# Performance work log

Hardware: AMD Instinct MI355X
Metric: run time of the kernel (lower is better)

The kernel has to match this reference:

```python
import math
import jax, jax.numpy as jnp
import numpy as np

N = 20000      # nodes
E = 320000     # edges
D_IN = 256
D_OUT = 256
H = 8
DK = D_OUT // H  # 32


def setup_inputs() -> dict:
    key = jax.random.key(0)
    ks = jax.random.split(key, 16)
    h = jax.random.normal(ks[0], (N, D_IN), dtype=jnp.float32)
    src = jax.random.randint(ks[1], (E,), 0, N, dtype=jnp.int32)
    dst = jax.random.randint(ks[2], (E,), 0, N, dtype=jnp.int32)
    s = 1.0 / math.sqrt(D_IN)
    Wk = jax.random.uniform(ks[3], (D_OUT, D_IN), jnp.float32, -s, s)
    bk = jnp.zeros((D_OUT,), jnp.float32)
    Wq = jax.random.uniform(ks[4], (D_OUT, D_IN), jnp.float32, -s, s)
    bq = jnp.zeros((D_OUT,), jnp.float32)
    Wv = jax.random.uniform(ks[5], (D_OUT, D_IN), jnp.float32, -s, s)
    bv = jnp.zeros((D_OUT,), jnp.float32)
    so = 1.0 / math.sqrt(D_OUT)
    Wa = jax.random.uniform(ks[6], (D_OUT, D_OUT), jnp.float32, -so, so)
    ba = jnp.zeros((D_OUT,), jnp.float32)
    # xavier_uniform over [n_rel=1, H, DK, DK]; fan_in = fan_out = DK
    bound = math.sqrt(6.0 / (DK + DK))
    rel_att = jax.random.uniform(ks[7], (H, DK, DK), jnp.float32, -bound, bound)
    rel_msg = jax.random.uniform(ks[8], (H, DK, DK), jnp.float32, -bound, bound)
    rel_pri = jnp.ones((H,), jnp.float32)
    skip = jnp.ones((), jnp.float32)
    return {"h": h, "src": src, "dst": dst, "Wk": Wk, "bk": bk, "Wq": Wq,
            "bq": bq, "Wv": Wv, "bv": bv, "Wa": Wa, "ba": ba,
            "rel_att": rel_att, "rel_msg": rel_msg, "rel_pri": rel_pri,
            "skip": skip}


def reference(h, src, dst, Wk, bk, Wq, bq, Wv, bv, Wa, ba, rel_att, rel_msg, rel_pri, skip):
    n = h.shape[0]
    sqrt_dk = math.sqrt(DK)
    # per-node projections, [N, H, DK]
    k = (h @ Wk.T + bk).reshape(n, H, DK)
    q = (h @ Wq.T + bq).reshape(n, H, DK)
    v = (h @ Wv.T + bv).reshape(n, H, DK)
    # relation-specific transforms (single relation, index 0)
    k = jnp.einsum('nhd,hde->nhe', k, rel_att)
    v = jnp.einsum('nhd,hde->nhe', v, rel_msg)
    # edge-wise dot-product score: v_dot_u(q_dst, k_src) -> [E, H]
    score = jnp.einsum('ehd,ehd->eh', q[dst], k[src]) * rel_pri / sqrt_dk
    # edge softmax normalized by dst
    m = jax.ops.segment_max(score, dst, num_segments=n)          # [N, H]
    ex = jnp.exp(score - m[dst])
    z = jax.ops.segment_sum(ex, dst, num_segments=n)             # [N, H]
    attn = ex / z[dst]                                           # [E, H]
    # weighted message aggregation: sum_e attn * v_src -> [N, H, DK]
    agg = jax.ops.segment_sum(v[src] * attn[:, :, None], dst, num_segments=n)
    t = agg.reshape(n, D_OUT)
    trans = t @ Wa.T + ba                                        # dropout = eval identity
    alpha = jax.nn.sigmoid(skip)
    return trans * alpha + h * (1.0 - alpha)
```

## Files before the change

kernel.cpp:

```cpp
#include <hip/hip_runtime.h>
#include <hip/hip_bf16.h>
#include <math.h>


#define NN   20000
#define NE   320000
#define MPAD 20096
#define DSTRIDE 96

typedef unsigned short u16;
typedef unsigned char  u8;
typedef __bf16 bf16x8 __attribute__((ext_vector_type(8)));
typedef u16    u16x8  __attribute__((ext_vector_type(8)));
typedef float  f32x4  __attribute__((ext_vector_type(4)));

__device__ __forceinline__ float bf2f(u16 x) {
    union { float f; unsigned u; } c; c.u = ((unsigned)x) << 16; return c.f;
}
__device__ __forceinline__ u16 f2bf(float f) {
    union { float f; unsigned u; } c; c.f = f;
    unsigned r = c.u + 0x7fffu + ((c.u >> 16) & 1u);
    return (u16)(r >> 16);
}

#if __has_builtin(__builtin_amdgcn_cvt_pk_fp8_f32) && __has_builtin(__builtin_amdgcn_cvt_pk_f32_fp8)
#define HWFP8 1
#else
#define HWFP8 0
#endif

__device__ __forceinline__ u8 f2fp8(float x) {
#if HWFP8
    return (u8)(__builtin_amdgcn_cvt_pk_fp8_f32(x, x, 0, false) & 0xff);
#else
    if (x != x) return 0x7f;
    unsigned sg = (x < 0.f) ? 0x80u : 0u;
    float a = fabsf(x); if (a > 448.f) a = 448.f;
    if (a < 0.015625f) {
        int m = (int)rintf(a * 512.f);
        if (m > 7) return (u8)(sg | 0x08);
        return (u8)(sg | m);
    }
    int e; (void)frexpf(a, &e);
    int p = e - 1;
    float mant = a * exp2f((float)(-p));
    int m = (int)rintf((mant - 1.f) * 8.f);
    int ef = p + 7;
    if (m == 8) { m = 0; ef++; }
    if (ef > 15) { ef = 15; m = 6; }
    return (u8)(sg | (ef << 3) | m);
#endif
}

__device__ __forceinline__ void fp8x4_dec(unsigned w, float* o) {
#if HWFP8
    auto lo = __builtin_amdgcn_cvt_pk_f32_fp8(w, false);
    auto hi = __builtin_amdgcn_cvt_pk_f32_fp8(w, true);
    o[0] = lo[0]; o[1] = lo[1]; o[2] = hi[0]; o[3] = hi[1];
#else
    #pragma unroll
    for (int j = 0; j < 4; ++j) {
        u8 b = (w >> (8 * j)) & 0xff;
        unsigned e = (b >> 3) & 15, m = b & 7;
        float v;
        if (e) { union { unsigned u; float f; } c; c.u = ((e + 120) << 23) | (m << 20); v = c.f; }
        else v = (float)m * 0.001953125f;
        o[j] = (b & 0x80) ? -v : v;
    }
#endif
}

__device__ __forceinline__ float fast_exp2(float x) {
#if __has_builtin(__builtin_amdgcn_exp2f)
    return __builtin_amdgcn_exp2f(x);
#else
    return exp2f(x);
#endif
}

__global__ void prep0(const float* __restrict__ Wq, const float* __restrict__ bq,
                      const float* __restrict__ Wk, const float* __restrict__ bk,
                      const float* __restrict__ Wv, const float* __restrict__ bv,
                      const float* __restrict__ Wa,
                      const float* __restrict__ rel_att, const float* __restrict__ rel_msg,
                      const float* __restrict__ rel_pri,
                      u16* __restrict__ W_all, float* __restrict__ b_eff,
                      u16* __restrict__ Wa_bf, int* __restrict__ cnt)
{
    const int bid = blockIdx.x, t = threadIdx.x;
    if (bid < 20) {
        const int i = bid * 256 + t;
        if (i < 5024) *(int4*)(cnt + i * 4) = make_int4(0, 0, 0, 0);
    } else if (bid < 788) {
        const int row = bid - 20, col = t;
        float val;
        if (row < 256) {
            val = Wq[row * 256 + col];
            if (col == 0) b_eff[row] = bq[row];
        } else {
            const int i = row - 256, g = i >> 7, o = i & 127;
            const bool isk = (o < 64);
            const int d = 64 * g + (isk ? o : o - 64);
            const int hh = d >> 5, e = d & 31;
            if (isk) {
                const float s = rel_pri[hh] * 0.17677669529663687f * 1.4426950408889634f;
                float acc = 0.f;
                for (int dd = 0; dd < 32; ++dd)
                    acc += rel_att[hh * 1024 + dd * 32 + e] * Wk[(hh * 32 + dd) * 256 + col];
                val = acc * s;
                if (col == 0) {
                    float b = 0.f;
                    for (int dd = 0; dd < 32; ++dd) b += rel_att[hh * 1024 + dd * 32 + e] * bk[hh * 32 + dd];
                    b_eff[row] = b * s;
                }
            } else {
                float acc = 0.f;
                for (int dd = 0; dd < 32; ++dd)
                    acc += rel_msg[hh * 1024 + dd * 32 + e] * Wv[(hh * 32 + dd) * 256 + col];
                val = acc;
                if (col == 0) {
                    float b = 0.f;
                    for (int dd = 0; dd < 32; ++dd) b += rel_msg[hh * 1024 + dd * 32 + e] * bv[hh * 32 + dd];
                    b_eff[row] = b;
                }
            }
        }
        W_all[row * 256 + col] = f2bf(val);
    } else {
        const int idx = (bid - 788) * 256 + t;
        Wa_bf[idx] = f2bf(Wa[idx]);
    }
}

__global__ __launch_bounds__(256) void gemm_qkv(
    const float* __restrict__ h, const u16* __restrict__ B,
    const float* __restrict__ bias, const int* __restrict__ src, const int* __restrict__ dst,
    u16* __restrict__ qb, u8* __restrict__ kv8, int* __restrict__ cnt, u16* __restrict__ esrc)
{
    if (blockIdx.x >= 960) {
        const int e0 = ((blockIdx.x - 960) * 256 + threadIdx.x) * 4;
        if (e0 < NE) {
            const int4 d4 = *(const int4*)(dst + e0);
            const int4 s4 = *(const int4*)(src + e0);
            const int p0 = atomicAdd(&cnt[d4.x], 1);
            const int p1 = atomicAdd(&cnt[d4.y], 1);
            const int p2 = atomicAdd(&cnt[d4.z], 1);
            const int p3 = atomicAdd(&cnt[d4.w], 1);
            if (p0 < DSTRIDE) esrc[d4.x * DSTRIDE + p0] = (u16)s4.x;
            if (p1 < DSTRIDE) esrc[d4.y * DSTRIDE + p1] = (u16)s4.y;
            if (p2 < DSTRIDE) esrc[d4.z * DSTRIDE + p2] = (u16)s4.z;
            if (p3 < DSTRIDE) esrc[d4.w * DSTRIDE + p3] = (u16)s4.w;
        }
        return;
    }
    const int xcd = blockIdx.x & 7, slot = blockIdx.x >> 3;
    const int rb = (slot % 20) * 8 + xcd;
    const int cb = slot / 20;
    if (rb >= 157) return;
    __shared__ u16 LDS[128 * 128];
    u16* At = LDS;
    u16* Bt = LDS + 128 * 64;
    const int t = threadIdx.x;
    const int wave = t >> 6, lane = t & 63;
    const int row0 = rb * 128, col0 = cb * 128;
    const int wm = (wave >> 1) * 64, wn = (wave & 1) * 64;
    const int cl = lane & 15, rh = lane >> 4;
    const int srow = t >> 3;
    const int lchunk = t & 7;
    const int swz = srow & 7;

    f32x4 acc[4][4] = {};
    float4 a0[4], a1[4];
    u16x8 bz[4];

    auto LOAD = [&](int k0) {
        #pragma unroll
        for (int r = 0; r < 4; ++r) {
            const int grow = row0 + r * 32 + srow;
            if (grow < NN) {
                a0[r] = *(const float4*)(h + (size_t)grow * 256 + k0 + lchunk * 8);
                a1[r] = *(const float4*)(h + (size_t)grow * 256 + k0 + lchunk * 8 + 4);
            } else {
                a0[r] = make_float4(0.f, 0.f, 0.f, 0.f);
                a1[r] = make_float4(0.f, 0.f, 0.f, 0.f);
            }
            bz[r] = *(const u16x8*)(B + (size_t)(col0 + r * 32 + srow) * 256 + k0 + lchunk * 8);
        }
    };
    auto COMMIT = [&]() {
        #pragma unroll
        for (int r = 0; r < 4; ++r) {
            u16x8 w8;
            w8[0] = f2bf(a0[r].x); w8[1] = f2bf(a0[r].y); w8[2] = f2bf(a0[r].z); w8[3] = f2bf(a0[r].w);
            w8[4] = f2bf(a1[r].x); w8[5] = f2bf(a1[r].y); w8[6] = f2bf(a1[r].z); w8[7] = f2bf(a1[r].w);
            *(u16x8*)&At[(r * 32 + srow) * 64 + (lchunk ^ swz) * 8] = w8;
            *(u16x8*)&Bt[(r * 32 + srow) * 64 + (lchunk ^ swz) * 8] = bz[r];
        }
    };

    LOAD(0);
    COMMIT();
    __syncthreads();
    #pragma unroll
    for (int ki = 0; ki < 4; ++ki) {
        if (ki < 3) LOAD((ki + 1) * 64);
        #pragma unroll
        for (int kk = 0; kk < 2; ++kk) {
            const int kc = kk * 4;
            bf16x8 af[4], bb[4];
            #pragma unroll
            for (int m = 0; m < 4; ++m) {
                const int ar = wm + 16 * m + cl;
                af[m] = *(const bf16x8*)&At[ar * 64 + (((kc + rh) ^ (ar & 7)) * 8)];
            }
            #pragma unroll
            for (int n = 0; n < 4; ++n) {
                const int br = wn + 16 * n + cl;
                bb[n] = *(const bf16x8*)&Bt[br * 64 + (((kc + rh) ^ (br & 7)) * 8)];
            }
            #pragma unroll
            for (int m = 0; m < 4; ++m)
                #pragma unroll
                for (int n = 0; n < 4; ++n)
                    acc[m][n] = __builtin_amdgcn_mfma_f32_16x16x32_bf16(af[m], bb[n], acc[m][n], 0, 0, 0);
        }
        __syncthreads();
        if (ki < 3) {
            COMMIT();
            __syncthreads();
        }
    }

    if (cb < 2) {
        #pragma unroll
        for (int n = 0; n < 4; ++n) {
            const int col = wn + 16 * n + cl;
            const float bv = bias[col0 + col];
            #pragma unroll
            for (int m = 0; m < 4; ++m) {
                const int rowb = wm + 16 * m + 4 * rh;
                #pragma unroll
                for (int r = 0; r < 4; ++r) {
                    const int row = rowb + r;
                    LDS[row * 128 + ((((col >> 3) ^ (row & 15)) << 3) | (col & 7))] =
                        f2bf(acc[m][n][r] + bv);
                }
            }
        }
        __syncthreads();
        #pragma unroll
        for (int it = 0; it < 8; ++it) {
            const int u = it * 256 + t;
            const int row = u >> 4, lc = u & 15;
            *(u16x8*)(qb + (size_t)(row0 + row) * 256 + col0 + lc * 8) =
                *(const u16x8*)&LDS[row * 128 + ((lc ^ (row & 15)) << 3)];
        }
    } else {
        u8* Cs8 = (u8*)LDS;
        const int g = cb - 2;
        #pragma unroll
        for (int n = 0; n < 4; ++n) {
            const int col = wn + 16 * n + cl;
            const float bv = bias[col0 + col];
            const int o = col & 63;
            const int p = ((o >> 3) << 4) + ((col < 64) ? 0 : 8) + (o & 7);
            #pragma unroll
            for (int m = 0; m < 4; ++m) {
                const int rowb = wm + 16 * m + 4 * rh;
                #pragma unroll
                for (int r = 0; r < 4; ++r) {
                    const int row = rowb + r;
                    Cs8[row * 128 + ((((p >> 3) ^ (row & 15)) << 3) | (p & 7))] =
                        f2fp8(acc[m][n][r] + bv);
                }
            }
        }
        __syncthreads();
        #pragma unroll
        for (int it = 0; it < 4; ++it) {
            const int u = it * 256 + t;
            const int row = u >> 3, un = u & 7;
            const uint2 a = *(const uint2*)&Cs8[row * 128 + (((2 * un) ^ (row & 15)) << 3)];
            const uint2 b = *(const uint2*)&Cs8[row * 128 + (((2 * un + 1) ^ (row & 15)) << 3)];
            *(uint4*)(kv8 + (size_t)(row0 + row) * 512 + g * 128 + un * 16) =
                make_uint4(a.x, a.y, b.x, b.y);
        }
    }
}

__global__ __launch_bounds__(256) void gemm_out(
    const u16* __restrict__ A, const u16* __restrict__ B,
    const float* __restrict__ bias, const float* __restrict__ hres,
    const float* __restrict__ skip, float* __restrict__ C)
{
    const int xcd = blockIdx.x & 7, slot = blockIdx.x >> 3;
    const int rb = (slot % 40) * 8 + xcd;
    const int cbo = slot / 40;
    if (rb >= 314) return;
    __shared__ u16 At[64 * 64];
    __shared__ u16 Bt[64 * 64];
    const int t = threadIdx.x;
    const int wave = t >> 6, lane = t & 63;
    const int row0 = rb * 64, col0 = cbo * 64;
    const int wm = (wave >> 1) * 32, wn = (wave & 1) * 32;
    const int cl = lane & 15, rh = lane >> 4;
    const int srow = t >> 3;
    const int lchunk = t & 7;
    const int swz = srow & 7;

    f32x4 acc[2][2] = {};
    u16x8 az[2], bz[2];

    auto LOAD = [&](int k0) {
        #pragma unroll
        for (int r = 0; r < 2; ++r) {
            az[r] = *(const u16x8*)(A + (size_t)(row0 + r * 32 + srow) * 256 + k0 + lchunk * 8);
            bz[r] = *(const u16x8*)(B + (size_t)(col0 + r * 32 + srow) * 256 + k0 + lchunk * 8);
        }
    };
    auto COMMIT = [&]() {
        #pragma unroll
        for (int r = 0; r < 2; ++r) {
            *(u16x8*)&At[(r * 32 + srow) * 64 + (lchunk ^ swz) * 8] = az[r];
            *(u16x8*)&Bt[(r * 32 + srow) * 64 + (lchunk ^ swz) * 8] = bz[r];
        }
    };

    LOAD(0);
    COMMIT();
    __syncthreads();
    #pragma unroll
    for (int ki = 0; ki < 4; ++ki) {
        if (ki < 3) LOAD((ki + 1) * 64);
        #pragma unroll
        for (int kk = 0; kk < 2; ++kk) {
            const int kc = kk * 4;
            bf16x8 af[2], bb[2];
            #pragma unroll
            for (int m = 0; m < 2; ++m) {
                const int ar = wm + 16 * m + cl;
                af[m] = *(const bf16x8*)&At[ar * 64 + (((kc + rh) ^ (ar & 7)) * 8)];
            }
            #pragma unroll
            for (int n = 0; n < 2; ++n) {
                const int br = wn + 16 * n + cl;
                bb[n] = *(const bf16x8*)&Bt[br * 64 + (((kc + rh) ^ (br & 7)) * 8)];
            }
            #pragma unroll
            for (int m = 0; m < 2; ++m)
                #pragma unroll
                for (int n = 0; n < 2; ++n)
                    acc[m][n] = __builtin_amdgcn_mfma_f32_16x16x32_bf16(af[m], bb[n], acc[m][n], 0, 0, 0);
        }
        __syncthreads();
        if (ki < 3) {
            COMMIT();
            __syncthreads();
        }
    }
    const float alpha = 1.f / (1.f + __expf(-skip[0]));
    const float beta = 1.f - alpha;
    #pragma unroll
    for (int n = 0; n < 2; ++n) {
        const int col = col0 + wn + 16 * n + cl;
        const float bv = bias[col];
        #pragma unroll
        for (int m = 0; m < 2; ++m) {
            const int rowb = row0 + wm + 16 * m + 4 * rh;
            #pragma unroll
            for (int r = 0; r < 4; ++r) {
                const int row = rowb + r;
                if (row < NN)
                    C[(size_t)row * 256 + col] =
                        (acc[m][n][r] + bv) * alpha + hres[(size_t)row * 256 + col] * beta;
            }
        }
    }
}

__device__ __forceinline__ void agg_w(uint4 w, const float* qf, float& z, float* acc)
{
    float kf[8], vf[8];
    fp8x4_dec(w.x, kf); fp8x4_dec(w.y, kf + 4);
    float s = 0.f;
    #pragma unroll
    for (int j = 0; j < 8; ++j) s += qf[j] * kf[j];
    s += __shfl_xor(s, 1);
    s += __shfl_xor(s, 2);
    const float ex = fast_exp2(s);
    z += ex;
    fp8x4_dec(w.z, vf); fp8x4_dec(w.w, vf + 4);
    #pragma unroll
    for (int j = 0; j < 8; ++j) acc[j] += ex * vf[j];
}

__global__ __launch_bounds__(256) void aggregate(
    const u16* __restrict__ qb, const u8* __restrict__ kv8, const int* __restrict__ cnt,
    const u16* __restrict__ esrc, u16* __restrict__ tout)
{
    const int wid = blockIdx.x * 4 + (threadIdx.x >> 6);
    const int lane = threadIdx.x & 63;
    const int half = lane >> 5, sl = lane & 31;
    if (wid >= MPAD) return;
    if (wid >= NN) {
        if (half == 0) *(u16x8*)(tout + (size_t)wid * 256 + sl * 8) = (u16x8)0;
        return;
    }
    const u16x8 qv = *(const u16x8*)(qb + (size_t)wid * 256 + sl * 8);
    float qf[8];
    #pragma unroll
    for (int j = 0; j < 8; ++j) qf[j] = bf2f(qv[j]);
    float acc[8] = {0.f, 0.f, 0.f, 0.f, 0.f, 0.f, 0.f, 0.f};
    float z = 0.f;
    const int dcnt = min(cnt[wid], DSTRIDE);
    const int e0 = wid * DSTRIDE;
    for (int c0 = 0; c0 < dcnt; c0 += 64) {
        const int cn = min(64, dcnt - c0);
        const int jj = c0 + lane;
        const int myid = (jj < dcnt) ? (int)esrc[e0 + jj] : 0;
        const int nfull = cn & ~15;
        int i = 0;
        for (; i < nfull; i += 16) {
            int idv[8];
            uint4 wreg[8];
            #pragma unroll
            for (int j = 0; j < 8; ++j) idv[j] = __shfl(myid, i + 2 * j + half);
            #pragma unroll
            for (int j = 0; j < 8; ++j)
                wreg[j] = *(const uint4*)(kv8 + (size_t)idv[j] * 512 + sl * 16);
            #pragma unroll
            for (int j = 0; j < 8; ++j) agg_w(wreg[j], qf, z, acc);
        }
        for (; i < cn; i += 2) {
            const int ii = i + half;
            const int id = __shfl(myid, ii);
            if (ii < cn) {
                const uint4 w = *(const uint4*)(kv8 + (size_t)id * 512 + sl * 16);
                agg_w(w, qf, z, acc);
            }
        }
    }
    #pragma unroll
    for (int j = 0; j < 8; ++j) acc[j] += __shfl_xor(acc[j], 32);
    z += __shfl_xor(z, 32);
    if (half == 0) {
        const float rz = (z > 0.f) ? 1.f / z : 0.f;
        u16x8 o;
        #pragma unroll
        for (int j = 0; j < 8; ++j) o[j] = f2bf(acc[j] * rz);
        *(u16x8*)(tout + (size_t)wid * 256 + sl * 8) = o;
    }
}

extern "C" void kernel_launch(void* const* d_in, const int* in_sizes, int n_in,
                              void* d_out, int out_size, void* d_ws, size_t ws_size,
                              hipStream_t stream)
{
    const float* h   = (const float*)d_in[0];
    const int*   src = (const int*)d_in[1];
    const int*   dst = (const int*)d_in[2];
    const float* Wk  = (const float*)d_in[3];
    const float* bk  = (const float*)d_in[4];
    const float* Wq  = (const float*)d_in[5];
    const float* bq  = (const float*)d_in[6];
    const float* Wv  = (const float*)d_in[7];
    const float* bv  = (const float*)d_in[8];
    const float* Wa  = (const float*)d_in[9];
    const float* ba  = (const float*)d_in[10];
    const float* rel_att = (const float*)d_in[11];
    const float* rel_msg = (const float*)d_in[12];
    const float* rel_pri = (const float*)d_in[13];
    const float* skip    = (const float*)d_in[14];
    float* out = (float*)d_out;

    char* w = (char*)d_ws;
    u16*   W_all = (u16*)(w + 0);
    float* b_eff = (float*)(w + 393216);
    u16*   Wa_bf = (u16*)(w + 396288);
    u16*   qb    = (u16*)(w + 527360);
    u8*    kv8   = (u8*)(w + 10816512);
    u16*   t_bf  = (u16*)(w + 21105664);
    int*   cnt   = (int*)(w + 31394816);
    u16*   esrc  = (u16*)(w + 31475200);

    prep0<<<1044, 256, 0, stream>>>(Wq, bq, Wk, bk, Wv, bv, Wa,
                                    rel_att, rel_msg, rel_pri,
                                    W_all, b_eff, Wa_bf, cnt);
    gemm_qkv<<<960 + 313, 256, 0, stream>>>(h, W_all, b_eff, src, dst, qb, kv8, cnt, esrc);
    aggregate<<<MPAD / 4, 256, 0, stream>>>(qb, kv8, cnt, esrc, t_bf);
    gemm_out<<<1280, 256, 0, stream>>>(t_bf, Wa_bf, ba, h, skip, out);
}
```

Baseline: 89.26 us.

## Replace global-atomic edge bucketing with per-block LDS-atomic dst-range scans

Edge bucketing by destination now runs on 128 side blocks instead of 313. Each block owns a contiguous range of 157 destination nodes, scans every edge, and counts its own edges with LDS atomics before writing the final counts to global memory. This removes the global atomics and the separate zeroing of the count array in prep0. In exchange, every scan block reads the full src and dst arrays, which multiplies edge-list traffic about 128-fold through the cache and makes each block's serial loop long.

```diff
diff --git a/kernel.cpp b/kernel.cpp
--- a/kernel.cpp
+++ b/kernel.cpp
@@ -7,6 +7,7 @@
 #define NE   320000
 #define MPAD 20096
 #define DSTRIDE 96
+#define NSCAN 128
 
 typedef unsigned short u16;
 typedef unsigned char  u8;
@@ -85,14 +86,11 @@
                       const float* __restrict__ rel_att, const float* __restrict__ rel_msg,
                       const float* __restrict__ rel_pri,
                       u16* __restrict__ W_all, float* __restrict__ b_eff,
-                      u16* __restrict__ Wa_bf, int* __restrict__ cnt)
+                      u16* __restrict__ Wa_bf)
 {
     const int bid = blockIdx.x, t = threadIdx.x;
-    if (bid < 20) {
-        const int i = bid * 256 + t;
-        if (i < 5024) *(int4*)(cnt + i * 4) = make_int4(0, 0, 0, 0);
-    } else if (bid < 788) {
-        const int row = bid - 20, col = t;
+    if (bid < 768) {
+        const int row = bid, col = t;
         float val;
         if (row < 256) {
             val = Wq[row * 256 + col];
@@ -127,7 +125,7 @@
         }
         W_all[row * 256 + col] = f2bf(val);
     } else {
-        const int idx = (bid - 788) * 256 + t;
+        const int idx = (bid - 768) * 256 + t;
         Wa_bf[idx] = f2bf(Wa[idx]);
     }
 }
@@ -137,30 +135,45 @@
     const float* __restrict__ bias, const int* __restrict__ src, const int* __restrict__ dst,
     u16* __restrict__ qb, u8* __restrict__ kv8, int* __restrict__ cnt, u16* __restrict__ esrc)
 {
+    __shared__ u16 LDS[128 * 128];
+    const int t = threadIdx.x;
     if (blockIdx.x >= 960) {
-        const int e0 = ((blockIdx.x - 960) * 256 + threadIdx.x) * 4;
-        if (e0 < NE) {
+        const int sid = blockIdx.x - 960;
+        const int base = sid * 157;
+        int* lcnt = (int*)LDS;
+        if (t < 157) lcnt[t] = 0;
+        __syncthreads();
+        for (int e0 = t * 4; e0 < NE; e0 += 1024) {
             const int4 d4 = *(const int4*)(dst + e0);
             const int4 s4 = *(const int4*)(src + e0);
-            const int p0 = atomicAdd(&cnt[d4.x], 1);
-            const int p1 = atomicAdd(&cnt[d4.y], 1);
-            const int p2 = atomicAdd(&cnt[d4.z], 1);
-            const int p3 = atomicAdd(&cnt[d4.w], 1);
-            if (p0 < DSTRIDE) esrc[d4.x * DSTRIDE + p0] = (u16)s4.x;
-            if (p1 < DSTRIDE) esrc[d4.y * DSTRIDE + p1] = (u16)s4.y;
-            if (p2 < DSTRIDE) esrc[d4.z * DSTRIDE + p2] = (u16)s4.z;
-            if (p3 < DSTRIDE) esrc[d4.w * DSTRIDE + p3] = (u16)s4.w;
-        }
+            const int r0 = d4.x - base, r1 = d4.y - base, r2 = d4.z - base, r3 = d4.w - base;
+            if ((unsigned)r0 < 157u) {
+                const int p = atomicAdd(&lcnt[r0], 1);
+                if (p < DSTRIDE) esrc[d4.x * DSTRIDE + p] = (u16)s4.x;
+            }
+            if ((unsigned)r1 < 157u) {
+                const int p = atomicAdd(&lcnt[r1], 1);
+                if (p < DSTRIDE) esrc[d4.y * DSTRIDE + p] = (u16)s4.y;
+            }
+            if ((unsigned)r2 < 157u) {
+                const int p = atomicAdd(&lcnt[r2], 1);
+                if (p < DSTRIDE) esrc[d4.z * DSTRIDE + p] = (u16)s4.z;
+            }
+            if ((unsigned)r3 < 157u) {
+                const int p = atomicAdd(&lcnt[r3], 1);
+                if (p < DSTRIDE) esrc[d4.w * DSTRIDE + p] = (u16)s4.w;
+            }
+        }
+        __syncthreads();
+        if (t < 157 && base + t < NN) cnt[base + t] = lcnt[t];
         return;
     }
     const int xcd = blockIdx.x & 7, slot = blockIdx.x >> 3;
     const int rb = (slot % 20) * 8 + xcd;
     const int cb = slot / 20;
     if (rb >= 157) return;
-    __shared__ u16 LDS[128 * 128];
     u16* At = LDS;
     u16* Bt = LDS + 128 * 64;
-    const int t = threadIdx.x;
     const int wave = t >> 6, lane = t & 63;
     const int row0 = rb * 128, col0 = cb * 128;
     const int wm = (wave >> 1) * 64, wn = (wave & 1) * 64;
@@ -483,10 +496,10 @@
     int*   cnt   = (int*)(w + 31394816);
     u16*   esrc  = (u16*)(w + 31475200);
 
-    prep0<<<1044, 256, 0, stream>>>(Wq, bq, Wk, bk, Wv, bv, Wa,
+    prep0<<<1024, 256, 0, stream>>>(Wq, bq, Wk, bk, Wv, bv, Wa,
                                     rel_att, rel_msg, rel_pri,
-                                    W_all, b_eff, Wa_bf, cnt);
-    gemm_qkv<<<960 + 313, 256, 0, stream>>>(h, W_all, b_eff, src, dst, qb, kv8, cnt, esrc);
+                                    W_all, b_eff, Wa_bf);
+    gemm_qkv<<<960 + NSCAN, 256, 0, stream>>>(h, W_all, b_eff, src, dst, qb, kv8, cnt, esrc);
     aggregate<<<MPAD / 4, 256, 0, stream>>>(qb, kv8, cnt, esrc, t_bf);
     gemm_out<<<1280, 256, 0, stream>>>(t_bf, Wa_bf, ba, h, skip, out);
 }
```

New measurement: 199.1 us. +123.1%, slower.
